# Kernel tuning notes

Measured on AMD Instinct MI355X. Metric: run time of the kernel, lower is better.

The kernel has to match this reference:

```python
import jax, jax.numpy as jnp
import numpy as np

B, R, L, F, H = 65536, 12, 16, 8, 64  # batch, rss_dim, n_leds, led_feat_dim, head_dim

def setup_inputs() -> dict:
    key = jax.random.key(0)
    ks = jax.random.split(key, 20)
    p = lambda k, shp, s=0.1: (jax.random.normal(k, shp, dtype=jnp.float32) * s)
    return {
        "rss_t": jax.random.uniform(ks[0], (B, R, 1), dtype=jnp.float32),
        "led_features": jax.random.normal(ks[1], (B, L, F), dtype=jnp.float32),
        "led_positions": jax.random.normal(ks[2], (B, L, 3), dtype=jnp.float32),
        "prev_pos": jax.random.normal(ks[3], (B, 3), dtype=jnp.float32),
        "freq_mask": jax.random.randint(ks[4], (R, L), 0, 2).astype(jnp.int32),
        # intensity_gate: Linear(1,16) -> ReLU -> Linear(16,1) -> Sigmoid
        "gw1": p(ks[5], (1, 16)), "gb1": p(ks[6], (16,)),
        "gw2": p(ks[7], (16, 1)), "gb2": p(ks[8], (1,)),
        # query_proj: Linear(1,32) -> ReLU -> Linear(32,64)
        "qw1": p(ks[9], (1, 32)), "qb1": p(ks[10], (32,)),
        "qw2": p(ks[11], (32, H)), "qb2": p(ks[12], (H,)),
        # key_proj: Linear(F+3,32) -> ReLU -> Linear(32,64)
        "kw1": p(ks[13], (F + 3, 32)), "kb1": p(ks[14], (32,)),
        "kw2": p(ks[15], (32, H)), "kb2": p(ks[16], (H,)),
        "sigma": jnp.float32(0.5),
    }

def reference(rss_t, led_features, led_positions, prev_pos, freq_mask,
              gw1, gb1, gw2, gb2, qw1, qb1, qw2, qb2, kw1, kb1, kw2, kb2, sigma):
    # intensity gate with hard threshold
    gate = jax.nn.sigmoid(jax.nn.relu(rss_t @ gw1 + gb1) @ gw2 + gb2)  # [B,R,1]
    iw = (rss_t > 0.5).astype(rss_t.dtype) * gate                      # [B,R,1]
    # query / key projections
    Q = jax.nn.relu((rss_t * iw) @ qw1 + qb1) @ qw2 + qb2              # [B,R,H]
    led_input = jnp.concatenate([led_features, led_positions], axis=-1)  # [B,L,F+3]
    K = jax.nn.relu(led_input @ kw1 + kb1) @ kw2 + kb2                 # [B,L,H]
    scores = jnp.einsum("brh,blh->brl", Q, K)                          # [B,R,L]
    # distance bias
    dist_sq = jnp.sum((prev_pos[:, None, :] - led_positions) ** 2, axis=-1)  # [B,L]
    scores = scores - dist_sq[:, None, :] / (2.0 * sigma ** 2)
    # mask + softmax
    neg = jnp.finfo(scores.dtype).min
    scores = jnp.where(freq_mask[None, :, :] == 0, neg, scores)
    attn = jax.nn.softmax(scores, axis=-1)                             # [B,R,L]
    return attn, iw.squeeze(-1)
```

## Files before the change

### kernel.cpp

```cpp
#include <hip/hip_runtime.h>

#define B_TOT 65536
#define R 12
#define L 16
#define NB 16
#define NEG_MIN -3.402823466e38f

#define WS_V   0
#define WS_C   32
#define WS_PM  40
#define WS_BP  64
#define WS_TAB 96
#define TROW   72
#define WS_WF  2472

typedef __attribute__((ext_vector_type(8))) short short8;
typedef __attribute__((ext_vector_type(4))) float f32x4;

static __device__ __forceinline__ short f2bf(float f) {
    uint32_t u = __float_as_uint(f);
    uint32_t r = u + 0x7FFFu + ((u >> 16) & 1u);
    return (short)(r >> 16);
}

static __device__ __forceinline__ unsigned cvt_pk_bf16(float a, float b) {
    unsigned d;
    asm("v_cvt_pk_bf16_f32 %0, %1, %2" : "=v"(d) : "v"(a), "v"(b));
    return d;
}

__global__ __launch_bounds__(256) void nfh_pre(
    const float* __restrict__ qw1, const float* __restrict__ qb1,
    const float* __restrict__ qw2, const float* __restrict__ qb2,
    const float* __restrict__ kw2, const float* __restrict__ kb2,
    const float* __restrict__ kw1, const float* __restrict__ kb1,
    const int*   __restrict__ fmask,
    float* __restrict__ ws)
{
    __shared__ float sM[1024];
    __shared__ float su[32];
    __shared__ float sw1[32], sb1[32], sbp[32], sbq[32];
    const int t = threadIdx.x;

    if (t < 32) { sw1[t] = qw1[t]; sb1[t] = qb1[t]; }
    for (int e = t; e < 1024; e += 256) {
        const int i = e >> 5, j = e & 31;
        float acc = 0.f;
        for (int h = 0; h < 64; ++h) acc = fmaf(qw2[i * 64 + h], kw2[j * 64 + h], acc);
        sM[e] = acc;
    }
    if (t < 32) {
        float au = 0.f, av = 0.f;
        for (int h = 0; h < 64; ++h) {
            au = fmaf(qw2[t * 64 + h], kb2[h], au);
            av = fmaf(kw2[t * 64 + h], qb2[h], av);
        }
        su[t] = au;
        ws[WS_V + t] = av;
        const float w = qw1[t];
        sbp[t] = (w != 0.f) ? (-qb1[t] / w) : 3.0e30f;
    }
    if (t == 64) {
        float acc = 0.f;
        for (int h = 0; h < 64; ++h) acc = fmaf(qb2[h], kb2[h], acc);
        ws[WS_C] = acc;
    }
    if (t < 12) {
        int pm = 0;
        for (int l = 0; l < 16; ++l) if (fmask[t * 16 + l] != 0) pm |= (1 << l);
        ((int*)ws)[WS_PM + t] = pm;
    }
    __syncthreads();
    if (t < 32) {
        const float key = sbp[t];
        int rank = 0;
        #pragma unroll
        for (int i = 0; i < 32; ++i) {
            const float vi = sbp[i];
            rank += (vi < key || (vi == key && i < t)) ? 1 : 0;
        }
        sbq[rank] = key;
    }
    __syncthreads();
    if (t < 32) ws[WS_BP + t] = sbq[t];

    for (int task = t; task < 33 * 32 + 33; task += 256) {
        const int m = (task < 33 * 32) ? (task >> 5) : (task - 33 * 32);
        const float xi = (m == 0) ? sbq[0] - 1.f
                       : ((m == 32) ? sbq[31] + 1.f
                                    : sbq[m - 1] + 0.5f * (sbq[m] - sbq[m - 1]));
        if (task < 33 * 32) {
            const int j = task & 31;
            float A = 0.f, Bv = 0.f;
            for (int i = 0; i < 32; ++i) {
                if (fmaf(sw1[i], xi, sb1[i]) > 0.f) {
                    A  = fmaf(sw1[i], sM[i * 32 + j], A);
                    Bv = fmaf(sb1[i], sM[i * 32 + j], Bv);
                }
            }
            ws[WS_TAB + m * TROW + j] = A;
            ws[WS_TAB + m * TROW + 36 + j] = Bv;
        } else {
            float Au = 0.f, Bu = 0.f;
            for (int i = 0; i < 32; ++i) {
                if (fmaf(sw1[i], xi, sb1[i]) > 0.f) {
                    Au = fmaf(sw1[i], su[i], Au);
                    Bu = fmaf(sb1[i], su[i], Bu);
                }
            }
            ws[WS_TAB + m * TROW + 32] = Au;
            ws[WS_TAB + m * TROW + 36 + 32] = Bu;
        }
    }

    {
        const int fr = t >> 6;
        const int li = t & 63;
        const int jl = li & 15, kb = li >> 4;
        const int T = fr & 1, term = fr >> 1;
        const int q = ((jl >> 2) << 3) + (T << 2) + (jl & 3);
        short* wsp = (short*)(ws + WS_WF);
        #pragma unroll
        for (int e = 0; e < 8; ++e) {
            const int k = kb * 8 + e;
            float w = 0.f;
            if (term == 0) {
                if (k < 11)       w = kw1[k * 32 + q];
                else if (k == 11) w = kb1[q];
            } else {
                if (k < 11)       w = kw1[k * 32 + q];
                else if (k == 11) { const float b = kb1[q];
                                    w = b - __uint_as_float(((uint32_t)(uint16_t)f2bf(b)) << 16); }
                else if (k < 23)  { const float a = kw1[(k - 12) * 32 + q];
                                    w = a - __uint_as_float(((uint32_t)(uint16_t)f2bf(a)) << 16); }
            }
            wsp[(fr * 64 + li) * 8 + e] = f2bf(w);
        }
    }
}

__global__ __launch_bounds__(256, 4) void nfh_main(
    const float* __restrict__ rss,
    const float* __restrict__ feat,
    const float* __restrict__ pos,
    const float* __restrict__ prev,
    const float* __restrict__ gw1, const float* __restrict__ gb1,
    const float* __restrict__ gw2, const float* __restrict__ gb2,
    const float* __restrict__ sigma_p,
    const float* __restrict__ ws,
    float* __restrict__ out)
{
    __shared__ short s_in[NB * 16 * 40 + 8];
    __shared__ short s_ttf[NB * 384];
    __shared__ float s_dq[NB * 16];
    __shared__ float s_tc[NB * 12];
    __shared__ int   s_pm[16];

    const int t = threadIdx.x;
    const int lane = t & 63;
    const int lg = lane >> 4;
    const int b0 = blockIdx.x * NB;
    const float sigma = sigma_p[0];
    const float inv2s2 = 1.f / (2.f * sigma * sigma);

    const short* wsp = (const short*)(ws + WS_WF);
    const short8 wf0 = *(const short8*)(wsp + (0 * 64 + lane) * 8);
    const short8 wf1 = *(const short8*)(wsp + (1 * 64 + lane) * 8);
    const short8 wf2 = *(const short8*)(wsp + (2 * 64 + lane) * 8);
    const short8 wf3 = *(const short8*)(wsp + (3 * 64 + lane) * 8);
    const f32x4 v0 = *(const f32x4*)(ws + WS_V + lg * 8);
    const f32x4 v1 = *(const f32x4*)(ws + WS_V + lg * 8 + 4);
    const float cconst = ws[WS_C];

    if (t < 16) s_pm[t] = (t < 12) ? ((const int*)ws)[WS_PM + t] : 0;
    if (t < 8)  s_in[NB * 16 * 40 + t] = 0;

    {
        const int bb1 = t >> 4, l1 = t & 15;
        const int b = b0 + bb1;
        float in[12];
        const float4* f4 = (const float4*)(feat + ((size_t)b * (L * 8) + l1 * 8));
        const float4 fa = f4[0], fb = f4[1];
        in[0] = fa.x; in[1] = fa.y; in[2] = fa.z; in[3] = fa.w;
        in[4] = fb.x; in[5] = fb.y; in[6] = fb.z; in[7] = fb.w;
        const float* pp = pos + ((size_t)b * (L * 3) + l1 * 3);
        in[8] = pp[0]; in[9] = pp[1]; in[10] = pp[2];
        in[11] = 1.0f;

        float dsq = 0.f;
        #pragma unroll
        for (int m = 0; m < 3; ++m) {
            const float d = prev[b * 3 + m] - in[8 + m];
            dsq = fmaf(d, d, dsq);
        }
        s_dq[bb1 * 16 + l1] = cconst - dsq * inv2s2;

        unsigned hp[6], lp[6];
        #pragma unroll
        for (int p = 0; p < 6; ++p) {
            const float a = in[2 * p], c = in[2 * p + 1];
            const unsigned h = cvt_pk_bf16(a, c);
            hp[p] = h;
            const float h0 = __uint_as_float(h << 16);
            const float h1 = __uint_as_float(h & 0xFFFF0000u);
            lp[p] = cvt_pk_bf16(a - h0, c - h1);
        }
        const unsigned lp5m = (lp[5] & 0xFFFFu) | 0x3F800000u;

        uint4* rowp = (uint4*)&s_in[(bb1 * 16 + l1) * 40];
        rowp[0] = make_uint4(hp[0], hp[1], hp[2], hp[3]);
        rowp[1] = make_uint4(hp[4], hp[5], 0u, 0u);
        rowp[2] = make_uint4(lp[0], lp[1], lp[2], lp[3]);
        rowp[3] = make_uint4(lp[4], lp5m, hp[0], hp[1]);
        rowp[4] = make_uint4(hp[2], hp[3], hp[4], hp[5] & 0xFFFFu);
    }

    if (t < NB * R) {
        const int bb2 = t / R;
        const int r2 = t - bb2 * R;
        const float x = rss[(size_t)b0 * R + t];
        float z = gb2[0];
        #pragma unroll
        for (int i = 0; i < 16; ++i) {
            const float h = fmaxf(fmaf(x, gw1[i], gb1[i]), 0.f);
            z = fmaf(h, gw2[i], z);
        }
        const float gate = 1.f / (1.f + __expf(-z));
        const float iw = (x > 0.5f) ? gate : 0.f;
        out[(size_t)B_TOT * R * L + (size_t)b0 * R + t] = iw;
        const float xq = x * iw;

        int k = 0;
        #pragma unroll
        for (int m = 0; m < 32; ++m) k += (xq > ws[WS_BP + m]) ? 1 : 0;
        const float* row = ws + WS_TAB + k * TROW;
        const float4* ra = (const float4*)row;
        const float4* rb = (const float4*)(row + 36);
        s_tc[bb2 * 12 + r2] = fmaf(xq, row[32], row[68]);
        #pragma unroll
        for (int kb = 0; kb < 4; ++kb) {
            const float4 a0 = ra[kb * 2], c0 = rb[kb * 2];
            const float4 a1 = ra[kb * 2 + 1], c1 = rb[kb * 2 + 1];
            uint4 pk;
            pk.x = cvt_pk_bf16(fmaf(xq, a0.x, c0.x), fmaf(xq, a0.y, c0.y));
            pk.y = cvt_pk_bf16(fmaf(xq, a0.z, c0.z), fmaf(xq, a0.w, c0.w));
            pk.z = cvt_pk_bf16(fmaf(xq, a1.x, c1.x), fmaf(xq, a1.y, c1.y));
            pk.w = cvt_pk_bf16(fmaf(xq, a1.z, c1.z), fmaf(xq, a1.w, c1.w));
            *(uint4*)&s_ttf[bb2 * 384 + (kb * 12 + r2) * 8] = pk;
        }
    }
    __syncthreads();

    {
        const int r = lane & 15;
        const int w = t >> 6;
        const int pm = s_pm[r];

        #pragma unroll
        for (int i = 0; i < 4; ++i) {
            const int bb = w * 4 + i;
            const short* rowb = &s_in[(bb * 16 + r) * 40];
            const short8 i1 = *(const short8*)(rowb + lg * 8);
            const short8 i2 = *(const short8*)(rowb + 16 + lg * 8);

            f32x4 d0 = {0.f, 0.f, 0.f, 0.f};
            f32x4 d1 = {0.f, 0.f, 0.f, 0.f};
            d0 = __builtin_amdgcn_mfma_f32_16x16x32_bf16(wf0, i1, d0, 0, 0, 0);
            d0 = __builtin_amdgcn_mfma_f32_16x16x32_bf16(wf2, i2, d0, 0, 0, 0);
            d1 = __builtin_amdgcn_mfma_f32_16x16x32_bf16(wf1, i1, d1, 0, 0, 0);
            d1 = __builtin_amdgcn_mfma_f32_16x16x32_bf16(wf3, i2, d1, 0, 0, 0);

            float vbp = 0.f;
            #pragma unroll
            for (int j = 0; j < 4; ++j) {
                d0[j] = fmaxf(d0[j], 0.f);
                vbp = fmaf(v0[j], d0[j], vbp);
            }
            #pragma unroll
            for (int j = 0; j < 4; ++j) {
                d1[j] = fmaxf(d1[j], 0.f);
                vbp = fmaf(v1[j], d1[j], vbp);
            }
            vbp += __shfl_xor(vbp, 16);
            vbp += __shfl_xor(vbp, 32);
            const float vbl = vbp + s_dq[bb * 16 + r];

            uint4 afp;
            afp.x = cvt_pk_bf16(d0[0], d0[1]);
            afp.y = cvt_pk_bf16(d0[2], d0[3]);
            afp.z = cvt_pk_bf16(d1[0], d1[1]);
            afp.w = cvt_pk_bf16(d1[2], d1[3]);
            const short8 af = *(const short8*)&afp;

            short8 bf = (short8){0, 0, 0, 0, 0, 0, 0, 0};
            float tc = 0.f;
            if (r < R) {
                bf = *(const short8*)&s_ttf[bb * 384 + (lg * 12 + r) * 8];
                tc = s_tc[bb * 12 + r];
            }
            f32x4 acc = {0.f, 0.f, 0.f, 0.f};
            acc = __builtin_amdgcn_mfma_f32_16x16x32_bf16(af, bf, acc, 0, 0, 0);

            float sc[4];
            #pragma unroll
            for (int j = 0; j < 4; ++j) {
                const float vbj = __shfl(vbl, lg * 4 + j);
                sc[j] = acc[j] + tc + vbj;
                if (!((pm >> (lg * 4 + j)) & 1)) sc[j] = NEG_MIN;
            }
            float mx = fmaxf(fmaxf(sc[0], sc[1]), fmaxf(sc[2], sc[3]));
            mx = fmaxf(mx, __shfl_xor(mx, 16));
            mx = fmaxf(mx, __shfl_xor(mx, 32));
            float sum = 0.f;
            #pragma unroll
            for (int j = 0; j < 4; ++j) { sc[j] = __expf(sc[j] - mx); sum += sc[j]; }
            sum += __shfl_xor(sum, 16);
            sum += __shfl_xor(sum, 32);
            const float inv = 1.f / sum;

            if (r < R) {
                float4* op = (float4*)(out + ((size_t)(b0 + bb) * R + r) * L + lg * 4);
                *op = make_float4(sc[0] * inv, sc[1] * inv, sc[2] * inv, sc[3] * inv);
            }
        }
    }
}

extern "C" void kernel_launch(void* const* d_in, const int* in_sizes, int n_in,
                              void* d_out, int out_size, void* d_ws, size_t ws_size,
                              hipStream_t stream) {
    const float* rss   = (const float*)d_in[0];
    const float* feat  = (const float*)d_in[1];
    const float* pos   = (const float*)d_in[2];
    const float* prev  = (const float*)d_in[3];
    const int*   fmask = (const int*)d_in[4];
    const float* gw1   = (const float*)d_in[5];
    const float* gb1   = (const float*)d_in[6];
    const float* gw2   = (const float*)d_in[7];
    const float* gb2   = (const float*)d_in[8];
    const float* qw1   = (const float*)d_in[9];
    const float* qb1   = (const float*)d_in[10];
    const float* qw2   = (const float*)d_in[11];
    const float* qb2   = (const float*)d_in[12];
    const float* kw1   = (const float*)d_in[13];
    const float* kb1   = (const float*)d_in[14];
    const float* kw2   = (const float*)d_in[15];
    const float* kb2   = (const float*)d_in[16];
    const float* sigma = (const float*)d_in[17];
    float* out = (float*)d_out;
    float* ws  = (float*)d_ws;

    nfh_pre<<<1, 256, 0, stream>>>(qw1, qb1, qw2, qb2, kw2, kb2, kw1, kb1, fmask, ws);
    nfh_main<<<B_TOT / NB, 256, 0, stream>>>(
        rss, feat, pos, prev,
        gw1, gb1, gw2, gb2,
        sigma, ws, out);
}
```

Baseline: 167.1 us.

## Make each wave own its batch rows and drop block-wide barrier

Halves the block to 128 threads with 8 batches per block and repartitions the staging so that each wave writes and reads only its own 4 batches in shared memory. The __syncthreads is replaced by a wave-local lgkmcnt wait, and the per-row mask is read straight from the workspace instead of being staged in shared memory. This aims to remove the cross-wave barrier stall and shrink per-block LDS. The cost is twice as many blocks and correctness that now depends on wave-local ordering of LDS accesses.

Measured after the change: 172.0 us. 1.03x slower.

```diff
diff --git a/kernel.cpp b/kernel.cpp
--- a/kernel.cpp
+++ b/kernel.cpp
@@ -3,7 +3,7 @@
 #define B_TOT 65536
 #define R 12
 #define L 16
-#define NB 16
+#define NB 8
 #define NEG_MIN -3.402823466e38f
 
 #define WS_V   0
@@ -13,6 +13,8 @@
 #define WS_TAB 96
 #define TROW   72
 #define WS_WF  2472
+
+#define WROWS (4 * 16 * 40 + 8)
 
 typedef __attribute__((ext_vector_type(8))) short short8;
 typedef __attribute__((ext_vector_type(4))) float f32x4;
@@ -139,7 +141,7 @@
     }
 }
 
-__global__ __launch_bounds__(256, 4) void nfh_main(
+__global__ __launch_bounds__(128, 4) void nfh_main(
     const float* __restrict__ rss,
     const float* __restrict__ feat,
     const float* __restrict__ pos,
@@ -150,14 +152,14 @@
     const float* __restrict__ ws,
     float* __restrict__ out)
 {
-    __shared__ short s_in[NB * 16 * 40 + 8];
+    __shared__ short s_in[2 * WROWS];
     __shared__ short s_ttf[NB * 384];
     __shared__ float s_dq[NB * 16];
     __shared__ float s_tc[NB * 12];
-    __shared__ int   s_pm[16];
 
     const int t = threadIdx.x;
     const int lane = t & 63;
+    const int wv = t >> 6;
     const int lg = lane >> 4;
     const int b0 = blockIdx.x * NB;
     const float sigma = sigma_p[0];
@@ -172,8 +174,7 @@
     const f32x4 v1 = *(const f32x4*)(ws + WS_V + lg * 8 + 4);
     const float cconst = ws[WS_C];
 
-    if (t < 16) s_pm[t] = (t < 12) ? ((const int*)ws)[WS_PM + t] : 0;
-    if (t < 8)  s_in[NB * 16 * 40 + t] = 0;
+    if (lane < 8) s_in[wv * WROWS + 4 * 16 * 40 + lane] = 0;
 
     {
         const int bb1 = t >> 4, l1 = t & 15;
@@ -207,7 +208,7 @@
         }
         const unsigned lp5m = (lp[5] & 0xFFFFu) | 0x3F800000u;
 
-        uint4* rowp = (uint4*)&s_in[(bb1 * 16 + l1) * 40];
+        uint4* rowp = (uint4*)&s_in[wv * WROWS + ((bb1 & 3) * 16 + l1) * 40];
         rowp[0] = make_uint4(hp[0], hp[1], hp[2], hp[3]);
         rowp[1] = make_uint4(hp[4], hp[5], 0u, 0u);
         rowp[2] = make_uint4(lp[0], lp[1], lp[2], lp[3]);
@@ -215,10 +216,11 @@
         rowp[4] = make_uint4(hp[2], hp[3], hp[4], hp[5] & 0xFFFFu);
     }
 
-    if (t < NB * R) {
-        const int bb2 = t / R;
-        const int r2 = t - bb2 * R;
-        const float x = rss[(size_t)b0 * R + t];
+    if ((t & 15) < R) {
+        const int bb2 = t >> 4;
+        const int r2 = t & 15;
+        const int b = b0 + bb2;
+        const float x = rss[(size_t)b * R + r2];
         float z = gb2[0];
         #pragma unroll
         for (int i = 0; i < 16; ++i) {
@@ -227,7 +229,7 @@
         }
         const float gate = 1.f / (1.f + __expf(-z));
         const float iw = (x > 0.5f) ? gate : 0.f;
-        out[(size_t)B_TOT * R * L + (size_t)b0 * R + t] = iw;
+        out[(size_t)B_TOT * R * L + (size_t)b * R + r2] = iw;
         const float xq = x * iw;
 
         int k = 0;
@@ -249,17 +251,17 @@
             *(uint4*)&s_ttf[bb2 * 384 + (kb * 12 + r2) * 8] = pk;
         }
     }
-    __syncthreads();
+
+    asm volatile("s_waitcnt lgkmcnt(0)" ::: "memory");
 
     {
         const int r = lane & 15;
-        const int w = t >> 6;
-        const int pm = s_pm[r];
+        const int pm = (r < R) ? ((const int*)ws)[WS_PM + r] : 0;
 
         #pragma unroll
         for (int i = 0; i < 4; ++i) {
-            const int bb = w * 4 + i;
-            const short* rowb = &s_in[(bb * 16 + r) * 40];
+            const int bb = wv * 4 + i;
+            const short* rowb = &s_in[wv * WROWS + (i * 16 + r) * 40];
             const short8 i1 = *(const short8*)(rowb + lg * 8);
             const short8 i2 = *(const short8*)(rowb + 16 + lg * 8);
 
@@ -351,7 +353,7 @@
     float* ws  = (float*)d_ws;
 
     nfh_pre<<<1, 256, 0, stream>>>(qw1, qb1, qw2, qb2, kw2, kb2, kw1, kb1, fmask, ws);
-    nfh_main<<<B_TOT / NB, 256, 0, stream>>>(
+    nfh_main<<<B_TOT / NB, 128, 0, stream>>>(
         rss, feat, pos, prev,
         gw1, gb1, gw2, gb2,
         sigma, ws, out);
```
